# Optimization experiments

Measured on AMD Instinct MI355X. Metric: run time of the kernel, lower is better.

The kernel has to match this reference:

```python
import jax, jax.numpy as jnp
import numpy as np

DIM = 256
HEADS = 8
DHEAD = 64
MEM = 4
HID = HEADS * DHEAD  # 512


def setup_inputs() -> dict:
    key = jax.random.key(0)
    k1, k2, k3, k4 = jax.random.split(key, 4)
    x = jax.random.normal(k1, (2, DIM, 48, 48), jnp.float32)
    gamma = jnp.zeros((DIM, 1, 1), jnp.float32)  # nn.Parameter init is zeros
    mem_kv = jax.random.normal(k2, (2, HEADS, MEM, DHEAD), jnp.float32)
    w_qkv = jax.random.normal(k3, (3 * HID, DIM), jnp.float32) * 0.05  # 1x1 conv weight
    w_out = jax.random.normal(k4, (DIM, HID), jnp.float32) * 0.05     # 1x1 conv weight
    return {"x": x, "gamma": gamma, "mem_kv": mem_kv, "w_qkv": w_qkv, "w_out": w_out}


def reference(x, gamma, mem_kv, w_qkv, w_out):
    b, c, h, w = x.shape
    scale = DHEAD ** -0.5
    # RMSNorm: F.normalize along channel dim (L2, eps=1e-12) * (gamma+1) * sqrt(dim)
    l2 = jnp.sqrt(jnp.sum(x * x, axis=1, keepdims=True))
    xn = x / jnp.maximum(l2, 1e-12) * (gamma + 1.0) * (c ** 0.5)
    # 1x1 conv to qkv: [b, 3*HID, h, w]
    qkv = jnp.einsum('oc,bchw->bohw', w_qkv, xn)
    qkv = qkv.reshape(b, 3, HEADS, DHEAD, h * w)
    # (b, heads, n, dhead)
    q = jnp.swapaxes(qkv[:, 0], 2, 3)
    k = jnp.swapaxes(qkv[:, 1], 2, 3)
    v = jnp.swapaxes(qkv[:, 2], 2, 3)
    # prepend learnable memory kv tokens
    mk = jnp.broadcast_to(mem_kv[0], (b, HEADS, MEM, DHEAD))
    mv = jnp.broadcast_to(mem_kv[1], (b, HEADS, MEM, DHEAD))
    k = jnp.concatenate([mk, k], axis=2)
    v = jnp.concatenate([mv, v], axis=2)
    sim = jnp.einsum('bhid,bhjd->bhij', q * scale, k)
    attn = jax.nn.softmax(sim, axis=-1)
    out = jnp.einsum('bhij,bhjd->bhid', attn, v)
    out = jnp.swapaxes(out, 2, 3).reshape(b, HID, h, w)
    return jnp.einsum('oc,bchw->bohw', w_out, out)
```

## Files before the change

### kernel.cpp

```cpp
#include <hip/hip_runtime.h>

#define BATCH 2
#define CDIM 256
#define NPIX 2304
#define NHEAD 8
#define DH 64
#define HID 512
#define NMEM 4
#define NKV 2308
#define NKVP 2368
#define QSCALE 0.125f
#define LOG2E 1.4426950408889634f
#define WQKV_E 393216
#define WOUT_E 131072
#define KVSPLIT 1216

typedef float f32x4 __attribute__((ext_vector_type(4)));
typedef __bf16 bf16x8 __attribute__((ext_vector_type(8)));
typedef unsigned short u16;
typedef u16 u16x4 __attribute__((ext_vector_type(4)));
typedef u16 u16x8 __attribute__((ext_vector_type(8)));
typedef unsigned u32x2 __attribute__((ext_vector_type(2)));

#if __has_builtin(__builtin_amdgcn_exp2f)
#define EXP2(x) __builtin_amdgcn_exp2f(x)
#else
#define EXP2(x) exp2f(x)
#endif

static __device__ __forceinline__ u16 f2b(float f) {
  union { float f; unsigned u; } a; a.f = f;
  unsigned u = a.u;
  u += 0x7fffu + ((u >> 16) & 1u);
  return (u16)(u >> 16);
}

__global__ __launch_bounds__(256) void k_prep(
    const float* __restrict__ wqkv, const float* __restrict__ wout,
    const float* __restrict__ gamma, const float* __restrict__ mem_kv,
    u16* __restrict__ wb, u16* __restrict__ kk, u16* __restrict__ vT)
{
  const int blk = blockIdx.x, t = threadIdx.x;
  if (blk < 256) {
    const int i0 = (blk * 256 + t) * 8;
    u16x8 o;
    if (i0 < WQKV_E) {
      const float sc = ((i0 >> 8) < 512) ? QSCALE * LOG2E : 1.0f;
      const int c0 = i0 & 255;
      const f32x4 a = *(const f32x4*)&wqkv[i0];
      const f32x4 b = *(const f32x4*)&wqkv[i0 + 4];
      const f32x4 g0 = *(const f32x4*)&gamma[c0];
      const f32x4 g1 = *(const f32x4*)&gamma[c0 + 4];
#pragma unroll
      for (int e = 0; e < 4; ++e) {
        o[e]     = f2b(a[e] * sc * (1.0f + g0[e]));
        o[e + 4] = f2b(b[e] * sc * (1.0f + g1[e]));
      }
    } else {
      const f32x4 a = *(const f32x4*)&wout[i0 - WQKV_E];
      const f32x4 b = *(const f32x4*)&wout[i0 - WQKV_E + 4];
#pragma unroll
      for (int e = 0; e < 4; ++e) { o[e] = f2b(a[e]); o[e + 4] = f2b(b[e]); }
    }
    *(u16x8*)&wb[i0] = o;
  } else if (blk < 272) {
    const int idx = (blk - 256) * 256 + t;
    const int d = idx & 63;
    const int m = (idx >> 6) & 3;
    const int h = (idx >> 8) & 7;
    const int b = idx >> 11;
    const float mk = mem_kv[((size_t)h * NMEM + m) * DH + d];
    const float mv = mem_kv[(((size_t)NHEAD + h) * NMEM + m) * DH + d];
    kk[(((size_t)(b * NHEAD + h)) * NKV + m) * DH + d] = f2b(mk);
    vT[(((size_t)(b * NHEAD + h)) * DH + d) * NKVP + m] = f2b(mv);
  } else {
    const int gid = (blk - 272) * 256 + t;
    const int row = gid >> 4;
    const int c0 = (gid & 15) * 4 + 2304;
    u16x4 z = {0, 0, 0, 0};
    *(u16x4*)&vT[(size_t)row * NKVP + c0] = z;
  }
}

__global__ __launch_bounds__(256) void k_norm(
    const float* __restrict__ x, u16* __restrict__ xnT)
{
  __shared__ float xs[16 * 261];
  __shared__ float red[16][17];
  __shared__ float rsh[16];
  const int t = threadIdx.x;
  const int blk = blockIdx.x;
  const int b = blk / 144;
  const int p0 = (blk % 144) * 16;
  const int px = t & 15, cg = t >> 4;
  const float* xb = x + (size_t)b * CDIM * NPIX + p0 + px;
  float ssq = 0.f;
#pragma unroll
  for (int i = 0; i < 16; ++i) {
    const int c = cg * 16 + i;
    const float v = xb[(size_t)c * NPIX];
    xs[px * 261 + c] = v;
    ssq += v * v;
  }
  red[px][cg] = ssq;
  __syncthreads();
  if (t < 16) {
    float s = 0.f;
#pragma unroll
    for (int i = 0; i < 16; ++i) s += red[t][i];
    rsh[t] = 16.0f / fmaxf(sqrtf(s), 1e-12f);
  }
  __syncthreads();
  {
    const int pp = t >> 4, c0 = (t & 15) * 16;
    const float rs = rsh[pp];
    u16x8 o0, o1;
#pragma unroll
    for (int e = 0; e < 8; ++e) {
      o0[e] = f2b(xs[pp * 261 + c0 + e] * rs);
      o1[e] = f2b(xs[pp * 261 + c0 + 8 + e] * rs);
    }
    u16* dst = &xnT[(size_t)(b * NPIX + p0 + pp) * CDIM + c0];
    *(u16x8*)dst = o0;
    *(u16x8*)(dst + 8) = o1;
  }
}

__global__ __launch_bounds__(256) void k_qkv(
    const u16* __restrict__ xnT, const u16* __restrict__ wb,
    u16* __restrict__ q, u16* __restrict__ kk, u16* __restrict__ vT)
{
  __shared__ __align__(16) u16 bs[64 * 256];
  const int t = threadIdx.x, w = t >> 6, l = t & 63, li = l & 15, kg = l >> 4;
  const int m0 = blockIdx.x * 64 + w * 16;
  const int n0 = blockIdx.y * 64;
  {
    const int brow = t >> 2, bcs = (t & 3) * 64;
    const int bsw = (brow & 7) * 8;
    const u16* wsrc = wb + (size_t)(n0 + brow) * CDIM + bcs;
#pragma unroll
    for (int j = 0; j < 8; ++j) {
      const u16x8 v = *(const u16x8*)&wsrc[j * 8];
      *(u16x8*)&bs[brow * 256 + ((bcs + j * 8) ^ bsw)] = v;
    }
  }
  const u16* ap = xnT + (size_t)(m0 + li) * CDIM + kg * 8;
  const int lsw = (li & 7) * 8;
  f32x4 acc[4];
#pragma unroll
  for (int cf = 0; cf < 4; ++cf) { f32x4 z = {0.f,0.f,0.f,0.f}; acc[cf] = z; }
  __syncthreads();
#pragma unroll
  for (int ks = 0; ks < 8; ++ks) {
    const bf16x8 af = *(const bf16x8*)(ap + ks * 32);
#pragma unroll
    for (int cf = 0; cf < 4; ++cf) {
      const int row = cf * 16 + li;
      const bf16x8 bfr = *(const bf16x8*)&bs[row * 256 + ((ks * 32 + kg * 8) ^ lsw)];
      acc[cf] = __builtin_amdgcn_mfma_f32_16x16x32_bf16(af, bfr, acc[cf], 0, 0, 0);
    }
  }
  const int bb = (m0 >= NPIX) ? 1 : 0;
  const int plbase = m0 - bb * NPIX + kg * 4;
#pragma unroll
  for (int cf = 0; cf < 4; ++cf) {
    const int o0f = n0 + cf * 16;
    const int r = o0f >> 9, oo = o0f & 511, h = oo >> 6, d = (oo & 63) + li;
    if (r == 0) {
      u16* base = q + ((size_t)(bb * NHEAD + h) * NPIX + plbase) * DH + d;
#pragma unroll
      for (int rr = 0; rr < 4; ++rr) base[(size_t)rr * DH] = f2b(acc[cf][rr]);
    } else if (r == 1) {
      u16* base = kk + ((size_t)(bb * NHEAD + h) * NKV + NMEM + plbase) * DH + d;
#pragma unroll
      for (int rr = 0; rr < 4; ++rr) base[(size_t)rr * DH] = f2b(acc[cf][rr]);
    } else {
      u16x4 pk;
#pragma unroll
      for (int rr = 0; rr < 4; ++rr) pk[rr] = f2b(acc[cf][rr]);
      *(u16x4*)&vT[(((size_t)(bb * NHEAD + h)) * DH + d) * NKVP + NMEM + plbase] = pk;
    }
  }
}

__global__ __launch_bounds__(512) void k_attn(
    const u16* __restrict__ q, const u16* __restrict__ kk, const u16* __restrict__ vT,
    u16* __restrict__ aoB)
{
  __shared__ __align__(16) char smem[51200];
  u16* kbuf = (u16*)smem;
  u16* vbuf = (u16*)(smem + 16384);
  u16* ps   = (u16*)(smem + 32768);
  float* accbuf = (float*)smem;
  float* mlbuf  = (float*)(smem + 17152);
  const int t = threadIdx.x;
  const int w = t >> 6, l = t & 63;
  const int qsub = w & 3, hf = w >> 2;
  const int li = l & 15, kg = l >> 4;
  const int id = blockIdx.x;
  const int xcd = id & 7, slot = id >> 3;
  const int yl = (slot >= 36) ? 1 : 0;
  const int xq = slot - yl * 36;
  const int bh = xcd * 2 + yl;
  const int b = bh >> 3, hh = bh & 7;
  const int qrow0 = xq * 64 + qsub * 16;
  const u16* qp = q + ((size_t)bh * NPIX + qrow0) * DH;
  const u16* kp = kk + (size_t)bh * NKV * DH;
  const u16* vp = vT + (size_t)bh * DH * NKVP;

  const bf16x8 bq0 = *(const bf16x8*)&qp[li * DH + kg * 8];
  const bf16x8 bq1 = *(const bf16x8*)&qp[li * DH + 32 + kg * 8];

  const int hft = t >> 8;
  const int tt = t & 255;
  const int srow = tt >> 3;
  const int scol = (tt & 7) * 8;
  const int ssw = (srow & 7) * 8;
  const int sbase = hft * KVSPLIT;
  u16* kdst0 = &kbuf[hft * 4096 + srow * 64 + (scol ^ ssw)];
  u16* kdst1 = &kbuf[hft * 4096 + (srow + 32) * 64 + (scol ^ ssw)];
  u16* vdst0 = &vbuf[hft * 4096 + srow * 64 + (scol ^ ssw)];
  u16* vdst1 = &vbuf[hft * 4096 + (srow + 32) * 64 + (scol ^ ssw)];

  f32x4 acc[4];
#pragma unroll
  for (int df = 0; df < 4; ++df) { f32x4 z = {0.f,0.f,0.f,0.f}; acc[df] = z; }
  float m = -1e30f, lsum = 0.f;
  const int cbase0 = hf * KVSPLIT;

  u16x8 rk0, rk1, rv0, rv1;
  rk0 = *(const u16x8*)&kp[(size_t)(sbase + srow) * DH + scol];
  rk1 = *(const u16x8*)&kp[(size_t)(sbase + srow + 32) * DH + scol];
  rv0 = *(const u16x8*)&vp[(size_t)srow * NKVP + sbase + scol];
  rv1 = *(const u16x8*)&vp[(size_t)(srow + 32) * NKVP + sbase + scol];

  const int NT = 19;
  for (int i = 0; i < NT; ++i) {
    __syncthreads();
    *(u16x8*)kdst0 = rk0;
    *(u16x8*)kdst1 = rk1;
    *(u16x8*)vdst0 = rv0;
    *(u16x8*)vdst1 = rv1;
    if (i + 1 < NT) {
      int nb = sbase + (i + 1) * 64;
      int snb = (nb > NKVP - 64) ? (NKVP - 64) : nb;
      int kr0 = nb + srow;      if (kr0 > NKV - 1) kr0 = NKV - 1;
      int kr1 = nb + srow + 32; if (kr1 > NKV - 1) kr1 = NKV - 1;
      rk0 = *(const u16x8*)&kp[(size_t)kr0 * DH + scol];
      rk1 = *(const u16x8*)&kp[(size_t)kr1 * DH + scol];
      rv0 = *(const u16x8*)&vp[(size_t)srow * NKVP + snb + scol];
      rv1 = *(const u16x8*)&vp[(size_t)(srow + 32) * NKVP + snb + scol];
    }
    __syncthreads();
    const int kbase = cbase0 + i * 64;
    if (kbase < NKV) {
      const bool lastt = (kbase + 64 > NKV);
      const u16* kb = &kbuf[hf * 4096];
      const u16* vb = &vbuf[hf * 4096];
      f32x4 s[4];
#pragma unroll
      for (int jf = 0; jf < 4; ++jf) {
        const int row = jf * 16 + li;
        const int rsw = (row & 7) * 8;
        const bf16x8 ak0 = *(const bf16x8*)&kb[row * 64 + ((kg * 8) ^ rsw)];
        const bf16x8 ak1 = *(const bf16x8*)&kb[row * 64 + ((32 + kg * 8) ^ rsw)];
        f32x4 sf = {0.f, 0.f, 0.f, 0.f};
        sf = __builtin_amdgcn_mfma_f32_16x16x32_bf16(ak0, bq0, sf, 0, 0, 0);
        sf = __builtin_amdgcn_mfma_f32_16x16x32_bf16(ak1, bq1, sf, 0, 0, 0);
        s[jf] = sf;
      }
      if (lastt) {
#pragma unroll
        for (int jf = 0; jf < 4; ++jf)
#pragma unroll
          for (int r = 0; r < 4; ++r)
            if (kbase + jf * 16 + kg * 4 + r >= NKV) s[jf][r] = -1e30f;
      }
      float pmax = fmaxf(fmaxf(fmaxf(s[0][0], s[0][1]), fmaxf(s[0][2], s[0][3])),
                         fmaxf(fmaxf(s[1][0], s[1][1]), fmaxf(s[1][2], s[1][3])));
      pmax = fmaxf(pmax, fmaxf(fmaxf(fmaxf(s[2][0], s[2][1]), fmaxf(s[2][2], s[2][3])),
                               fmaxf(fmaxf(s[3][0], s[3][1]), fmaxf(s[3][2], s[3][3]))));
      pmax = fmaxf(pmax, __shfl_xor(pmax, 16));
      pmax = fmaxf(pmax, __shfl_xor(pmax, 32));
      if (__any(pmax > m + 8.0f)) {
        const float mn = fmaxf(m, pmax);
        const float al = EXP2(m - mn);
        m = mn;
        lsum *= al;
        float a4[4];
#pragma unroll
        for (int r = 0; r < 4; ++r) a4[r] = __shfl(al, (l & 48) | (kg * 4 + r));
#pragma unroll
        for (int df = 0; df < 4; ++df)
#pragma unroll
          for (int r = 0; r < 4; ++r) acc[df][r] *= a4[r];
      }
#pragma unroll
      for (int jf = 0; jf < 4; ++jf) {
        u32x2 wp;
#pragma unroll
        for (int rp = 0; rp < 2; ++rp) {
          const float e0 = EXP2(s[jf][rp * 2 + 0] - m);
          const float e1 = EXP2(s[jf][rp * 2 + 1] - m);
          lsum += e0 + e1;
          unsigned pk;
          asm("v_cvt_pk_bf16_f32 %0, %1, %2" : "=v"(pk) : "v"(e0), "v"(e1));
          wp[rp] = pk;
        }
        *(u32x2*)&ps[w * 1152 + li * 72 + jf * 16 + kg * 4] = wp;
      }
      asm volatile("s_waitcnt lgkmcnt(0)" ::: "memory");
      __builtin_amdgcn_sched_barrier(0);
      const bf16x8 ap0 = *(const bf16x8*)&ps[w * 1152 + li * 72 + kg * 8];
      const bf16x8 ap1 = *(const bf16x8*)&ps[w * 1152 + li * 72 + 32 + kg * 8];
#pragma unroll
      for (int df = 0; df < 4; ++df) {
        const int row = df * 16 + li;
        const int rsw = (row & 7) * 8;
        const bf16x8 bv0 = *(const bf16x8*)&vb[row * 64 + ((kg * 8) ^ rsw)];
        const bf16x8 bv1 = *(const bf16x8*)&vb[row * 64 + ((32 + kg * 8) ^ rsw)];
        acc[df] = __builtin_amdgcn_mfma_f32_16x16x32_bf16(ap0, bv0, acc[df], 0, 0, 0);
        acc[df] = __builtin_amdgcn_mfma_f32_16x16x32_bf16(ap1, bv1, acc[df], 0, 0, 0);
      }
    }
  }
  lsum += __shfl_xor(lsum, 16);
  lsum += __shfl_xor(lsum, 32);
  float m4[4], l4[4];
#pragma unroll
  for (int r = 0; r < 4; ++r) {
    const int src = (l & 48) | (kg * 4 + r);
    m4[r] = __shfl(m, src);
    l4[r] = __shfl(lsum, src);
  }
  __syncthreads();
  if (hf == 1) {
#pragma unroll
    for (int df = 0; df < 4; ++df)
#pragma unroll
      for (int r = 0; r < 4; ++r)
        accbuf[(qsub * 16 + kg * 4 + r) * 67 + df * 16 + li] = acc[df][r];
    if (kg == 0) {
      mlbuf[(qsub * 16 + li) * 2 + 0] = m;
      mlbuf[(qsub * 16 + li) * 2 + 1] = lsum;
    }
  }
  __syncthreads();
  if (hf == 0) {
    float f0[4], f1[4], rL[4];
#pragma unroll
    for (int r = 0; r < 4; ++r) {
      const float m1 = mlbuf[(qsub * 16 + kg * 4 + r) * 2 + 0];
      const float l1 = mlbuf[(qsub * 16 + kg * 4 + r) * 2 + 1];
      const float M = fmaxf(m4[r], m1);
      f0[r] = EXP2(m4[r] - M);
      f1[r] = EXP2(m1 - M);
      rL[r] = __builtin_amdgcn_rcpf(l4[r] * f0[r] + l1 * f1[r]);
    }
#pragma unroll
    for (int df = 0; df < 4; ++df)
#pragma unroll
      for (int r = 0; r < 4; ++r) {
        const float a1 = accbuf[(qsub * 16 + kg * 4 + r) * 67 + df * 16 + li];
        const float o = (acc[df][r] * f0[r] + a1 * f1[r]) * rL[r];
        aoB[((size_t)b * NPIX + qrow0 + kg * 4 + r) * HID + hh * DH + df * 16 + li] = f2b(o);
      }
  }
}

__global__ __launch_bounds__(256) void k_outg(
    const u16* __restrict__ aoB, const u16* __restrict__ wob, float* __restrict__ out)
{
  const int t = threadIdx.x, w = t >> 6, l = t & 63, li = l & 15, kg = l >> 4;
  const int wm = w >> 1, wn = w & 1;
  const int m0 = blockIdx.x * 32 + wm * 16;
  const int n0 = blockIdx.y * 32 + wn * 16;
  const u16* ap = aoB + (size_t)(m0 + li) * HID + kg * 8;
  const u16* bp = wob + (size_t)(n0 + li) * HID + kg * 8;
  f32x4 acc = {0.f, 0.f, 0.f, 0.f};
#pragma unroll
  for (int ks = 0; ks < 16; ++ks) {
    const bf16x8 af = *(const bf16x8*)(ap + ks * 32);
    const bf16x8 bf = *(const bf16x8*)(bp + ks * 32);
    acc = __builtin_amdgcn_mfma_f32_16x16x32_bf16(af, bf, acc, 0, 0, 0);
  }
  const int bb = (m0 >= NPIX) ? 1 : 0;
  const int pl = m0 - bb * NPIX + kg * 4;
  const int o = n0 + li;
  *(f32x4*)&out[((size_t)(bb * CDIM + o)) * NPIX + pl] = acc;
}

extern "C" void kernel_launch(void* const* d_in, const int* in_sizes, int n_in,
                              void* d_out, int out_size, void* d_ws, size_t ws_size,
                              hipStream_t stream)
{
  const float* x      = (const float*)d_in[0];
  const float* gamma  = (const float*)d_in[1];
  const float* mem_kv = (const float*)d_in[2];
  const float* wqkv   = (const float*)d_in[3];
  const float* wout   = (const float*)d_in[4];
  float* out = (float*)d_out;
  char* ws = (char*)d_ws;
  const size_t XNT = (size_t)BATCH * NPIX * CDIM * sizeof(u16);
  const size_t WB  = (size_t)(WQKV_E + WOUT_E) * sizeof(u16);
  const size_t QB  = (size_t)BATCH * NHEAD * NPIX * DH * sizeof(u16);
  const size_t KB  = (size_t)BATCH * NHEAD * NKV  * DH * sizeof(u16);
  const size_t VTB = (size_t)BATCH * NHEAD * DH * NKVP * sizeof(u16);
  u16* xnT = (u16*)ws;
  u16* wb  = (u16*)(ws + XNT);
  u16* q   = (u16*)(ws + XNT + WB);
  u16* kk  = (u16*)(ws + XNT + WB + QB);
  u16* vT  = (u16*)(ws + XNT + WB + QB + KB);
  u16* aoB = (u16*)(ws + XNT + WB + QB + KB + VTB);

  k_prep<<<dim3(336), dim3(256), 0, stream>>>(wqkv, wout, gamma, mem_kv, wb, kk, vT);
  k_norm<<<dim3(288), dim3(256), 0, stream>>>(x, xnT);
  k_qkv<<<dim3(72, 24), dim3(256), 0, stream>>>(xnT, wb, q, kk, vT);
  k_attn<<<dim3(576), dim3(512), 0, stream>>>(q, kk, vT, aoB);
  k_outg<<<dim3(144, 8), dim3(256), 0, stream>>>(aoB, wb + WQKV_E, out);
}
```

Before: 104.4 us.

## Fuse norm into prep kernel, enlarge GEMM tiles, stage out-proj weights in LDS

Merges the RMS-norm kernel into the prep kernel so one launch is removed. The QKV projection tile along N grows from 64 to 128, giving each block twice the MFMA work per A-fragment load. The output projection now stages a 64x512 weight tile in swizzled LDS, with each wave computing four output fragments. The attention loop moves its second barrier to sit before the global prefetch and is kept rolled with unroll 1. Larger tiles mean fewer blocks and more LDS per block, which may reduce occupancy, and the barrier move may expose global load latency.

After: 93.86 us. -10.1%, faster.

```diff
diff --git a/kernel.cpp b/kernel.cpp
--- a/kernel.cpp
+++ b/kernel.cpp
@@ -34,12 +34,20 @@
   u += 0x7fffu + ((u >> 16) & 1u);
   return (u16)(u >> 16);
 }
+static __device__ __forceinline__ float b2f(u16 b) {
+  union { float f; unsigned u; } a; a.u = ((unsigned)b) << 16; return a.f;
+}
 
 __global__ __launch_bounds__(256) void k_prep(
     const float* __restrict__ wqkv, const float* __restrict__ wout,
     const float* __restrict__ gamma, const float* __restrict__ mem_kv,
-    u16* __restrict__ wb, u16* __restrict__ kk, u16* __restrict__ vT)
+    const float* __restrict__ x,
+    u16* __restrict__ wb, u16* __restrict__ kk, u16* __restrict__ vT,
+    u16* __restrict__ xnT)
 {
+  __shared__ float xs[16 * 261];
+  __shared__ float red[16][17];
+  __shared__ float rsh[16];
   const int blk = blockIdx.x, t = threadIdx.x;
   if (blk < 256) {
     const int i0 = (blk * 256 + t) * 8;
@@ -73,56 +81,48 @@
     const float mv = mem_kv[(((size_t)NHEAD + h) * NMEM + m) * DH + d];
     kk[(((size_t)(b * NHEAD + h)) * NKV + m) * DH + d] = f2b(mk);
     vT[(((size_t)(b * NHEAD + h)) * DH + d) * NKVP + m] = f2b(mv);
-  } else {
+  } else if (blk < 336) {
     const int gid = (blk - 272) * 256 + t;
     const int row = gid >> 4;
     const int c0 = (gid & 15) * 4 + 2304;
     u16x4 z = {0, 0, 0, 0};
     *(u16x4*)&vT[(size_t)row * NKVP + c0] = z;
-  }
-}
-
-__global__ __launch_bounds__(256) void k_norm(
-    const float* __restrict__ x, u16* __restrict__ xnT)
-{
-  __shared__ float xs[16 * 261];
-  __shared__ float red[16][17];
-  __shared__ float rsh[16];
-  const int t = threadIdx.x;
-  const int blk = blockIdx.x;
-  const int b = blk / 144;
-  const int p0 = (blk % 144) * 16;
-  const int px = t & 15, cg = t >> 4;
-  const float* xb = x + (size_t)b * CDIM * NPIX + p0 + px;
-  float ssq = 0.f;
-#pragma unroll
-  for (int i = 0; i < 16; ++i) {
-    const int c = cg * 16 + i;
-    const float v = xb[(size_t)c * NPIX];
-    xs[px * 261 + c] = v;
-    ssq += v * v;
-  }
-  red[px][cg] = ssq;
-  __syncthreads();
-  if (t < 16) {
-    float s = 0.f;
-#pragma unroll
-    for (int i = 0; i < 16; ++i) s += red[t][i];
-    rsh[t] = 16.0f / fmaxf(sqrtf(s), 1e-12f);
-  }
-  __syncthreads();
-  {
-    const int pp = t >> 4, c0 = (t & 15) * 16;
-    const float rs = rsh[pp];
-    u16x8 o0, o1;
-#pragma unroll
-    for (int e = 0; e < 8; ++e) {
-      o0[e] = f2b(xs[pp * 261 + c0 + e] * rs);
-      o1[e] = f2b(xs[pp * 261 + c0 + 8 + e] * rs);
-    }
-    u16* dst = &xnT[(size_t)(b * NPIX + p0 + pp) * CDIM + c0];
-    *(u16x8*)dst = o0;
-    *(u16x8*)(dst + 8) = o1;
+  } else {
+    const int blk2 = blk - 336;
+    const int b = blk2 / 144;
+    const int p0 = (blk2 % 144) * 16;
+    const int px = t & 15, cg = t >> 4;
+    const float* xb = x + (size_t)b * CDIM * NPIX + p0 + px;
+    float ssq = 0.f;
+#pragma unroll
+    for (int i = 0; i < 16; ++i) {
+      const int c = cg * 16 + i;
+      const float v = xb[(size_t)c * NPIX];
+      xs[px * 261 + c] = v;
+      ssq += v * v;
+    }
+    red[px][cg] = ssq;
+    __syncthreads();
+    if (t < 16) {
+      float s = 0.f;
+#pragma unroll
+      for (int i = 0; i < 16; ++i) s += red[t][i];
+      rsh[t] = 16.0f / fmaxf(sqrtf(s), 1e-12f);
+    }
+    __syncthreads();
+    {
+      const int pp = t >> 4, c0 = (t & 15) * 16;
+      const float rs = rsh[pp];
+      u16x8 o0, o1;
+#pragma unroll
+      for (int e = 0; e < 8; ++e) {
+        o0[e] = f2b(xs[pp * 261 + c0 + e] * rs);
+        o1[e] = f2b(xs[pp * 261 + c0 + 8 + e] * rs);
+      }
+      u16* dst = &xnT[(size_t)(b * NPIX + p0 + pp) * CDIM + c0];
+      *(u16x8*)dst = o0;
+      *(u16x8*)(dst + 8) = o1;
+    }
   }
 }
 
@@ -130,31 +130,31 @@
     const u16* __restrict__ xnT, const u16* __restrict__ wb,
     u16* __restrict__ q, u16* __restrict__ kk, u16* __restrict__ vT)
 {
-  __shared__ __align__(16) u16 bs[64 * 256];
+  __shared__ __align__(16) u16 bs[128 * 256];
   const int t = threadIdx.x, w = t >> 6, l = t & 63, li = l & 15, kg = l >> 4;
   const int m0 = blockIdx.x * 64 + w * 16;
-  const int n0 = blockIdx.y * 64;
+  const int n0 = blockIdx.y * 128;
   {
-    const int brow = t >> 2, bcs = (t & 3) * 64;
+    const int brow = t >> 1, bcs = (t & 1) * 128;
     const int bsw = (brow & 7) * 8;
     const u16* wsrc = wb + (size_t)(n0 + brow) * CDIM + bcs;
 #pragma unroll
-    for (int j = 0; j < 8; ++j) {
+    for (int j = 0; j < 16; ++j) {
       const u16x8 v = *(const u16x8*)&wsrc[j * 8];
       *(u16x8*)&bs[brow * 256 + ((bcs + j * 8) ^ bsw)] = v;
     }
   }
   const u16* ap = xnT + (size_t)(m0 + li) * CDIM + kg * 8;
   const int lsw = (li & 7) * 8;
-  f32x4 acc[4];
-#pragma unroll
-  for (int cf = 0; cf < 4; ++cf) { f32x4 z = {0.f,0.f,0.f,0.f}; acc[cf] = z; }
+  f32x4 acc[8];
+#pragma unroll
+  for (int cf = 0; cf < 8; ++cf) { f32x4 z = {0.f,0.f,0.f,0.f}; acc[cf] = z; }
   __syncthreads();
 #pragma unroll
   for (int ks = 0; ks < 8; ++ks) {
     const bf16x8 af = *(const bf16x8*)(ap + ks * 32);
 #pragma unroll
-    for (int cf = 0; cf < 4; ++cf) {
+    for (int cf = 0; cf < 8; ++cf) {
       const int row = cf * 16 + li;
       const bf16x8 bfr = *(const bf16x8*)&bs[row * 256 + ((ks * 32 + kg * 8) ^ lsw)];
       acc[cf] = __builtin_amdgcn_mfma_f32_16x16x32_bf16(af, bfr, acc[cf], 0, 0, 0);
@@ -163,7 +163,7 @@
   const int bb = (m0 >= NPIX) ? 1 : 0;
   const int plbase = m0 - bb * NPIX + kg * 4;
 #pragma unroll
-  for (int cf = 0; cf < 4; ++cf) {
+  for (int cf = 0; cf < 8; ++cf) {
     const int o0f = n0 + cf * 16;
     const int r = o0f >> 9, oo = o0f & 511, h = oo >> 6, d = (oo & 63) + li;
     if (r == 0) {
@@ -235,12 +235,14 @@
   rv1 = *(const u16x8*)&vp[(size_t)(srow + 32) * NKVP + sbase + scol];
 
   const int NT = 19;
+#pragma unroll 1
   for (int i = 0; i < NT; ++i) {
     __syncthreads();
     *(u16x8*)kdst0 = rk0;
     *(u16x8*)kdst1 = rk1;
     *(u16x8*)vdst0 = rv0;
     *(u16x8*)vdst1 = rv1;
+    __syncthreads();
     if (i + 1 < NT) {
       int nb = sbase + (i + 1) * 64;
       int snb = (nb > NKVP - 64) ? (NKVP - 64) : nb;
@@ -251,7 +253,6 @@
       rv0 = *(const u16x8*)&vp[(size_t)srow * NKVP + snb + scol];
       rv1 = *(const u16x8*)&vp[(size_t)(srow + 32) * NKVP + snb + scol];
     }
-    __syncthreads();
     const int kbase = cbase0 + i * 64;
     if (kbase < NKV) {
       const bool lastt = (kbase + 64 > NKV);
@@ -371,23 +372,43 @@
 __global__ __launch_bounds__(256) void k_outg(
     const u16* __restrict__ aoB, const u16* __restrict__ wob, float* __restrict__ out)
 {
+  __shared__ __align__(16) u16 bs[64 * 512];
   const int t = threadIdx.x, w = t >> 6, l = t & 63, li = l & 15, kg = l >> 4;
-  const int wm = w >> 1, wn = w & 1;
-  const int m0 = blockIdx.x * 32 + wm * 16;
-  const int n0 = blockIdx.y * 32 + wn * 16;
+  const int m0 = blockIdx.x * 64 + w * 16;
+  const int n0 = blockIdx.y * 64;
+  {
+    const int brow = t >> 2, bcs = (t & 3) * 128;
+    const int bsw = (brow & 7) * 8;
+    const u16* wsrc = wob + (size_t)(n0 + brow) * HID + bcs;
+#pragma unroll
+    for (int j = 0; j < 16; ++j) {
+      const u16x8 v = *(const u16x8*)&wsrc[j * 8];
+      *(u16x8*)&bs[brow * 512 + ((bcs + j * 8) ^ bsw)] = v;
+    }
+  }
   const u16* ap = aoB + (size_t)(m0 + li) * HID + kg * 8;
-  const u16* bp = wob + (size_t)(n0 + li) * HID + kg * 8;
-  f32x4 acc = {0.f, 0.f, 0.f, 0.f};
+  const int lsw = (li & 7) * 8;
+  f32x4 acc[4];
+#pragma unroll
+  for (int cf = 0; cf < 4; ++cf) { f32x4 z = {0.f,0.f,0.f,0.f}; acc[cf] = z; }
+  __syncthreads();
 #pragma unroll
   for (int ks = 0; ks < 16; ++ks) {
     const bf16x8 af = *(const bf16x8*)(ap + ks * 32);
-    const bf16x8 bf = *(const bf16x8*)(bp + ks * 32);
-    acc = __builtin_amdgcn_mfma_f32_16x16x32_bf16(af, bf, acc, 0, 0, 0);
+#pragma unroll
+    for (int cf = 0; cf < 4; ++cf) {
+      const int row = cf * 16 + li;
+      const bf16x8 bf = *(const bf16x8*)&bs[row * 512 + ((ks * 32 + kg * 8) ^ lsw)];
+      acc[cf] = __builtin_amdgcn_mfma_f32_16x16x32_bf16(af, bf, acc[cf], 0, 0, 0);
+    }
   }
   const int bb = (m0 >= NPIX) ? 1 : 0;
   const int pl = m0 - bb * NPIX + kg * 4;
-  const int o = n0 + li;
-  *(f32x4*)&out[((size_t)(bb * CDIM + o)) * NPIX + pl] = acc;
+#pragma unroll
+  for (int cf = 0; cf < 4; ++cf) {
+    const int o = n0 + cf * 16 + li;
+    *(f32x4*)&out[((size_t)(bb * CDIM + o)) * NPIX + pl] = acc[cf];
+  }
 }
 
 extern "C" void kernel_launch(void* const* d_in, const int* in_sizes, int n_in,
@@ -413,9 +434,9 @@
   u16* vT  = (u16*)(ws + XNT + WB + QB + KB);
   u16* aoB = (u16*)(ws + XNT + WB + QB + KB + VTB);
 
-  k_prep<<<dim3(336), dim3(256), 0, stream>>>(wqkv, wout, gamma, mem_kv, wb, kk, vT);
-  k_norm<<<dim3(288), dim3(256), 0, stream>>>(x, xnT);
-  k_qkv<<<dim3(72, 24), dim3(256), 0, stream>>>(xnT, wb, q, kk, vT);
+  k_prep<<<dim3(624), dim3(256), 0, stream>>>(wqkv, wout, gamma, mem_kv, x,
+                                              wb, kk, vT, xnT);
+  k_qkv<<<dim3(72, 12), dim3(256), 0, stream>>>(xnT, wb, q, kk, vT);
   k_attn<<<dim3(576), dim3(512), 0, stream>>>(q, kk, vT, aoB);
-  k_outg<<<dim3(144, 8), dim3(256), 0, stream>>>(aoB, wb + WQKV_E, out);
-}
+  k_outg<<<dim3(72, 4), dim3(256), 0, stream>>>(aoB, wb + WQKV_E, out);
+}
```
